# Kernel optimization log

Hardware: AMD Instinct MI355X
Metric: run time of the kernel (lower is better)

The kernel has to match this reference:

```python
import jax, jax.numpy as jnp
import numpy as np

DIM = 768
NH = 12
HD = DIM // NH
MLP = 4 * DIM
EPS = 1e-5


def _ln(x, w, b):
    mu = x.mean(-1, keepdims=True)
    var = ((x - mu) ** 2).mean(-1, keepdims=True)
    return (x - mu) * jax.lax.rsqrt(var + EPS) * w + b


def setup_inputs() -> dict:
    key = jax.random.key(0)
    ks = jax.random.split(key, 12)
    s = 0.02
    return {
        "xq": jax.random.normal(ks[0], (4, 32, 32, DIM), jnp.float32),
        "xkv": jax.random.normal(ks[1], (4, 64, 64, DIM), jnp.float32),
        "norm1_w": jnp.ones((DIM,), jnp.float32),
        "norm1_b": jnp.zeros((DIM,), jnp.float32),
        "kv_w": jax.random.normal(ks[2], (DIM, 2 * DIM), jnp.float32) * s,
        "kv_b": jnp.zeros((2 * DIM,), jnp.float32),
        "q_w": jax.random.normal(ks[3], (DIM, DIM), jnp.float32) * s,
        "q_b": jnp.zeros((DIM,), jnp.float32),
        "proj_w": jax.random.normal(ks[4], (DIM, DIM), jnp.float32) * s,
        "proj_b": jnp.zeros((DIM,), jnp.float32),
        "norm2_w": jnp.ones((DIM,), jnp.float32),
        "norm2_b": jnp.zeros((DIM,), jnp.float32),
        "mlp_w1": jax.random.normal(ks[5], (DIM, MLP), jnp.float32) * s,
        "mlp_b1": jnp.zeros((MLP,), jnp.float32),
        "mlp_w2": jax.random.normal(ks[6], (MLP, DIM), jnp.float32) * s,
        "mlp_b2": jnp.zeros((DIM,), jnp.float32),
    }


def reference(xq, xkv, norm1_w, norm1_b, kv_w, kv_b, q_w, q_b, proj_w, proj_b,
              norm2_w, norm2_b, mlp_w1, mlp_b1, mlp_w2, mlp_b2):
    B, Hq, Wq, C = xq.shape
    _, H, W, _ = xkv.shape
    shortcut = xq
    xn = _ln(xq, norm1_w, norm1_b)
    # kv projection: [B, H*W, 2, NH, HD]
    kv = (xkv.reshape(B, H * W, C) @ kv_w + kv_b).reshape(B, H * W, 2, NH, HD)
    k = kv[:, :, 0].transpose(0, 2, 1, 3)  # [B, NH, HW, HD]
    v = kv[:, :, 1].transpose(0, 2, 1, 3)
    q = (xn.reshape(B, Hq * Wq, C) @ q_w + q_b).reshape(B, Hq * Wq, NH, HD).transpose(0, 2, 1, 3)
    scale = HD ** -0.5
    attn = jnp.einsum('bhqd,bhkd->bhqk', q * scale, k)
    attn = jax.nn.softmax(attn, axis=-1)
    o = jnp.einsum('bhqk,bhkd->bhqd', attn, v)  # [B, NH, HqWq, HD]
    o = o.transpose(0, 2, 1, 3).reshape(B, Hq, Wq, C)
    o = o @ proj_w + proj_b
    x = shortcut + o
    xn2 = _ln(x, norm2_w, norm2_b)
    mlp = jax.nn.gelu(xn2 @ mlp_w1 + mlp_b1, approximate=False) @ mlp_w2 + mlp_b2
    return x + mlp
```

## Files before the change

### kernel.cpp

```cpp
#include <hip/hip_runtime.h>
#include <hip/hip_bf16.h>
#include <math.h>

#define DIM 768
#define NH 12
#define HD 64
#define NQ 1024
#define NKV 4096
#define QSCALE 0.18033688011112042f

typedef __attribute__((ext_vector_type(4))) float f32x4;
typedef __attribute__((ext_vector_type(16))) float f32x16;
typedef __attribute__((ext_vector_type(8))) __bf16 bf16x8;
typedef __attribute__((ext_vector_type(8))) unsigned short u16x8;
typedef __attribute__((ext_vector_type(4))) unsigned short u16x4;
typedef unsigned short u16;

typedef const __attribute__((address_space(1))) void* gas_t;
typedef __attribute__((address_space(3))) void* las_t;

__device__ __forceinline__ void gl16(const void* g, void* l) {
    __builtin_amdgcn_global_load_lds((gas_t)g, (las_t)l, 16, 0, 0);
}

__device__ __forceinline__ u16 f2b(float x) {
    __bf16 h = (__bf16)x;
    return __builtin_bit_cast(u16, h);
}

__device__ __forceinline__ float b2f(u16 x) {
    unsigned int u = ((unsigned int)x) << 16;
    return __builtin_bit_cast(float, u);
}

__device__ __forceinline__ f32x4 mfma16(const u16* a, const u16* b, f32x4 c) {
    bf16x8 av = *reinterpret_cast<const bf16x8*>(a);
    bf16x8 bv = *reinterpret_cast<const bf16x8*>(b);
    return __builtin_amdgcn_mfma_f32_16x16x32_bf16(av, bv, c, 0, 0, 0);
}

__device__ __forceinline__ f32x16 mfma32(bf16x8 a, bf16x8 b, f32x16 c) {
    return __builtin_amdgcn_mfma_f32_32x32x16_bf16(a, b, c, 0, 0, 0);
}

__global__ __launch_bounds__(256) void cast_bf16_kernel(
    const float* __restrict__ in, u16* __restrict__ out, int n8)
{
    int i = blockIdx.x * 256 + threadIdx.x;
    if (i >= n8) return;
    const float4* p = reinterpret_cast<const float4*>(in) + (size_t)i * 2;
    float4 a = p[0], b = p[1];
    u16x8 o;
    o[0] = f2b(a.x); o[1] = f2b(a.y); o[2] = f2b(a.z); o[3] = f2b(a.w);
    o[4] = f2b(b.x); o[5] = f2b(b.y); o[6] = f2b(b.z); o[7] = f2b(b.w);
    reinterpret_cast<u16x8*>(out)[i] = o;
}

__global__ __launch_bounds__(256) void transpose_cast_kernel(
    const float* __restrict__ W, u16* __restrict__ Wt, int K, int N)
{
    __shared__ u16 T[64][72];
    int k0 = blockIdx.y * 64, n0 = blockIdx.x * 64;
    int tid = threadIdx.x;
    int r = tid >> 2, c = (tid & 3) * 16;
    const float* src = W + (size_t)(k0 + r) * N + n0 + c;
    #pragma unroll
    for (int j = 0; j < 16; j += 4) {
        float4 f = *reinterpret_cast<const float4*>(src + j);
        T[r][c + j + 0] = f2b(f.x); T[r][c + j + 1] = f2b(f.y);
        T[r][c + j + 2] = f2b(f.z); T[r][c + j + 3] = f2b(f.w);
    }
    __syncthreads();
    int d = tid >> 2, c2 = (tid & 3) * 16;
    u16x8 o0, o1;
    #pragma unroll
    for (int j = 0; j < 8; ++j) o0[j] = T[c2 + j][d];
    #pragma unroll
    for (int j = 0; j < 8; ++j) o1[j] = T[c2 + 8 + j][d];
    u16* dst = Wt + (size_t)(n0 + d) * K + k0 + c2;
    *reinterpret_cast<u16x8*>(dst) = o0;
    *reinterpret_cast<u16x8*>(dst + 8) = o1;
}

__global__ __launch_bounds__(256) void ln_kernel(
    const float* __restrict__ x, const float* __restrict__ w,
    const float* __restrict__ b, u16* __restrict__ out)
{
    int row = blockIdx.x;
    const float* xr = x + (size_t)row * DIM;
    int tid = threadIdx.x;
    float v0 = xr[tid], v1 = xr[tid + 256], v2 = xr[tid + 512];
    float s = v0 + v1 + v2;
    float s2 = v0 * v0 + v1 * v1 + v2 * v2;
    for (int off = 1; off < 64; off <<= 1) {
        s += __shfl_xor(s, off);
        s2 += __shfl_xor(s2, off);
    }
    __shared__ float ss[4], ss2[4];
    int wid = tid >> 6, lane = tid & 63;
    if (lane == 0) { ss[wid] = s; ss2[wid] = s2; }
    __syncthreads();
    s = ss[0] + ss[1] + ss[2] + ss[3];
    s2 = ss2[0] + ss2[1] + ss2[2] + ss2[3];
    float mu = s * (1.0f / DIM);
    float var = s2 * (1.0f / DIM) - mu * mu;
    float r = rsqrtf(var + 1e-5f);
    u16* orow = out + (size_t)row * DIM;
    orow[tid]       = f2b((v0 - mu) * r * w[tid]       + b[tid]);
    orow[tid + 256] = f2b((v1 - mu) * r * w[tid + 256] + b[tid + 256]);
    orow[tid + 512] = f2b((v2 - mu) * r * w[tid + 512] + b[tid + 512]);
}

template <int EPI>
__global__ __launch_bounds__(256) void gemm_kernel(
    const u16* __restrict__ A, const u16* __restrict__ Bt,
    const float* __restrict__ bias, const float* __restrict__ res,
    void* __restrict__ out, void* __restrict__ out2, int M, int N, int K)
{
    __shared__ u16 As[2][4096];
    __shared__ u16 Bs[2][4096];
    int p = blockIdx.x;
    int nbx = N >> 7;
    int ypx = (M >> 7) >> 3;
    int xcd = p & 7, slot = p >> 3;
    int by = xcd * ypx + slot / nbx;
    int bx = slot - (slot / nbx) * nbx;
    int n0 = bx * 128, m0 = by * 128;
    int tid = threadIdx.x, lane = tid & 63, wave = tid >> 6;
    int wm = (wave >> 1) * 64, wn = (wave & 1) * 64;
    f32x4 acc[4][4] = {};

    int ca = tid, cb = tid + 256;
    int ra = ca >> 2, sa = ((ca & 3) ^ (ra & 3)) * 8;
    int rb = cb >> 2, sb = ((cb & 3) ^ (rb & 3)) * 8;
    const u16* Asrc1 = A + (size_t)(m0 + ra) * K + sa;
    const u16* Asrc2 = A + (size_t)(m0 + rb) * K + sb;
    const u16* Bsrc1 = Bt + (size_t)(n0 + ra) * K + sa;
    const u16* Bsrc2 = Bt + (size_t)(n0 + rb) * K + sb;

    auto STAGE = [&](int buf, int k0) {
        gl16(Asrc1 + k0, &As[buf][ca * 8]);
        gl16(Asrc2 + k0, &As[buf][cb * 8]);
        gl16(Bsrc1 + k0, &Bs[buf][ca * 8]);
        gl16(Bsrc2 + k0, &Bs[buf][cb * 8]);
    };

    int fr = lane & 15, fq = lane >> 4;
    int co = (fq ^ (fr & 3)) * 8;

    auto COMPUTE = [&](int buf) {
        #pragma unroll
        for (int mf = 0; mf < 4; ++mf) {
            const u16* a = &As[buf][(wm + mf * 16 + fr) * 32 + co];
            #pragma unroll
            for (int nf = 0; nf < 4; ++nf)
                acc[mf][nf] = mfma16(a, &Bs[buf][(wn + nf * 16 + fr) * 32 + co],
                                     acc[mf][nf]);
        }
    };

    STAGE(0, 0);
    asm volatile("s_waitcnt vmcnt(0)" ::: "memory");
    __builtin_amdgcn_s_barrier();
    for (int k0 = 0; k0 < K; k0 += 64) {
        STAGE(1, k0 + 32);
        COMPUTE(0);
        asm volatile("s_waitcnt vmcnt(0)" ::: "memory");
        __builtin_amdgcn_s_barrier();
        if (k0 + 64 < K) STAGE(0, k0 + 64);
        COMPUTE(1);
        asm volatile("s_waitcnt vmcnt(0)" ::: "memory");
        __builtin_amdgcn_s_barrier();
    }

    if constexpr (EPI == 4) {
        u16* kb = reinterpret_cast<u16*>(out);
        u16* vtb = reinterpret_cast<u16*>(out2);
        if (n0 < 768) {
            #pragma unroll
            for (int mf = 0; mf < 4; ++mf)
                #pragma unroll
                for (int nf = 0; nf < 4; ++nf) {
                    int col = n0 + wn + nf * 16 + fr;
                    float bv = bias[col];
                    #pragma unroll
                    for (int r = 0; r < 4; ++r) {
                        int row = m0 + wm + mf * 16 + fq * 4 + r;
                        kb[(size_t)row * 768 + col] = f2b(acc[mf][nf][r] + bv);
                    }
                }
        } else {
            #pragma unroll
            for (int mf = 0; mf < 4; ++mf)
                #pragma unroll
                for (int nf = 0; nf < 4; ++nf) {
                    int col = n0 + wn + nf * 16 + fr;
                    int c = col - 768, h = c >> 6, d = c & 63;
                    float bv = bias[col];
                    int row0 = m0 + wm + mf * 16 + fq * 4;
                    int bb = row0 >> 12, kvi = row0 & 4095;
                    int kv6 = kvi & 63;
                    int slot = (kv6 & 51) | ((kv6 & 4) << 1) | ((kv6 & 8) >> 1);
                    u16x4 pv;
                    #pragma unroll
                    for (int r = 0; r < 4; ++r) pv[r] = f2b(acc[mf][nf][r] + bv);
                    *reinterpret_cast<u16x4*>(vtb + ((size_t)(bb * 12 + h) * 64 + d) * 4096
                                              + (kvi & ~63) + slot) = pv;
                }
        }
        return;
    }

    float* outf = reinterpret_cast<float*>(out);
    u16* outb = reinterpret_cast<u16*>(out);
    #pragma unroll
    for (int mf = 0; mf < 4; ++mf)
        #pragma unroll
        for (int nf = 0; nf < 4; ++nf)
            #pragma unroll
            for (int r = 0; r < 4; ++r) {
                int row = m0 + wm + mf * 16 + fq * 4 + r;
                int col = n0 + wn + nf * 16 + fr;
                size_t idx = (size_t)row * N + col;
                float v = acc[mf][nf][r] + bias[col];
                if constexpr (EPI == 2) {
                    outf[idx] = v + res[idx];
                } else {
                    float g = 0.5f * v * (1.0f + erff(v * 0.70710678118f));
                    outb[idx] = f2b(g);
                }
            }
}

template <int EPI>
__global__ __launch_bounds__(256) void gemm64_kernel(
    const u16* __restrict__ A, const u16* __restrict__ Bt,
    const float* __restrict__ bias, const float* __restrict__ res,
    void* __restrict__ out, int M, int N, int K)
{
    __shared__ u16 As[2][4096];
    __shared__ u16 Bs[2][4096];
    int p = blockIdx.x;
    int nbx = N >> 6;
    int ypx = (M >> 6) >> 3;
    int xcd = p & 7, slot = p >> 3;
    int by = xcd * ypx + slot / nbx;
    int bx = slot - (slot / nbx) * nbx;
    int n0 = bx * 64, m0 = by * 64;
    int tid = threadIdx.x, lane = tid & 63, wave = tid >> 6;
    int wm = (wave >> 1) * 32, wn = (wave & 1) * 32;
    f32x4 acc[2][2] = {};

    int c1 = tid, c2 = tid + 256;
    int r1 = c1 >> 3, s1 = ((c1 & 7) ^ (r1 & 7)) * 8;
    int r2 = c2 >> 3, s2 = ((c2 & 7) ^ (r2 & 7)) * 8;
    const u16* As1 = A + (size_t)(m0 + r1) * K + s1;
    const u16* As2 = A + (size_t)(m0 + r2) * K + s2;
    const u16* Bt1 = Bt + (size_t)(n0 + r1) * K + s1;
    const u16* Bt2 = Bt + (size_t)(n0 + r2) * K + s2;

    auto STAGE = [&](int buf, int k0) {
        gl16(As1 + k0, &As[buf][c1 * 8]);
        gl16(As2 + k0, &As[buf][c2 * 8]);
        gl16(Bt1 + k0, &Bs[buf][c1 * 8]);
        gl16(Bt2 + k0, &Bs[buf][c2 * 8]);
    };

    int fr = lane & 15, fq = lane >> 4;
    int co0 = (fq ^ (fr & 7)) * 8;
    int co1 = ((4 + fq) ^ (fr & 7)) * 8;

    STAGE(0, 0);
    asm volatile("s_waitcnt vmcnt(0)" ::: "memory");
    __builtin_amdgcn_s_barrier();
    int NIT = K >> 6;
    for (int it = 0; it < NIT; ++it) {
        int cur = it & 1;
        if (it + 1 < NIT) STAGE(cur ^ 1, (it + 1) << 6);
        #pragma unroll
        for (int mf = 0; mf < 2; ++mf) {
            const u16* arow = &As[cur][(wm + mf * 16 + fr) * 64];
            #pragma unroll
            for (int nf = 0; nf < 2; ++nf) {
                const u16* brow = &Bs[cur][(wn + nf * 16 + fr) * 64];
                acc[mf][nf] = mfma16(arow + co0, brow + co0, acc[mf][nf]);
                acc[mf][nf] = mfma16(arow + co1, brow + co1, acc[mf][nf]);
            }
        }
        asm volatile("s_waitcnt vmcnt(0)" ::: "memory");
        __builtin_amdgcn_s_barrier();
    }

    float* outf = reinterpret_cast<float*>(out);
    u16* outb = reinterpret_cast<u16*>(out);
    #pragma unroll
    for (int mf = 0; mf < 2; ++mf)
        #pragma unroll
        for (int nf = 0; nf < 2; ++nf)
            #pragma unroll
            for (int r = 0; r < 4; ++r) {
                int row = m0 + wm + mf * 16 + fq * 4 + r;
                int col = n0 + wn + nf * 16 + fr;
                size_t idx = (size_t)row * N + col;
                float v = acc[mf][nf][r] + bias[col];
                if constexpr (EPI == 1) {
                    outb[idx] = f2b(v * QSCALE);
                } else {
                    outf[idx] = v + res[idx];
                }
            }
}

__global__ __launch_bounds__(256, 4) void attn_kernel(
    const u16* __restrict__ q, const u16* __restrict__ kbuf,
    const u16* __restrict__ vt, u16* __restrict__ op0, u16* __restrict__ op1,
    u16* __restrict__ op2, u16* __restrict__ op3, float* __restrict__ L)
{
    int p = blockIdx.x;
    int xcd = p & 7, slot = p >> 3;
    int bh = xcd * 6 + (slot >> 5);
    int rem = slot & 31;
    int qt = rem >> 2, quarter = rem & 3;
    int h = bh % NH, bb = bh / NH;
    const int NIT = 16;

    __shared__ u16 Kb[2][4096];
    __shared__ u16 Vb[2][4096];

    int tid = threadIdx.x, lane = tid & 63, wave = tid >> 6;
    int l31 = lane & 31, hi = lane >> 5;
    int sw = l31 & 7;

    u16x8 ov = {0x3F80, 0x3F80, 0x3F80, 0x3F80, 0x3F80, 0x3F80, 0x3F80, 0x3F80};
    const bf16x8 ONES = __builtin_bit_cast(bf16x8, ov);

    bf16x8 qf[4];
    {
        const u16* qbp = q + (size_t)(bb * NQ + qt * 128 + wave * 32 + l31) * DIM
                         + h * HD + hi * 8;
        #pragma unroll
        for (int ks = 0; ks < 4; ++ks)
            qf[ks] = *reinterpret_cast<const bf16x8*>(qbp + ks * 16);
    }

    int c1 = tid, c2 = tid + 256;
    int r1 = c1 >> 3, sc1 = (c1 & 7) ^ (r1 & 7);
    int r2 = c2 >> 3, sc2 = (c2 & 7) ^ (r2 & 7);
    size_t krow0 = (size_t)bb * NKV + quarter * 1024;
    const u16* ks1 = kbuf + (krow0 + r1) * 768 + h * HD + sc1 * 8;
    const u16* ks2 = kbuf + (krow0 + r2) * 768 + h * HD + sc2 * 8;
    const u16* vs1 = vt + ((size_t)bh * HD + r1) * NKV + quarter * 1024 + sc1 * 8;
    const u16* vs2 = vt + ((size_t)bh * HD + r2) * NKV + quarter * 1024 + sc2 * 8;

    auto STAGE = [&](int buf, int kv0) {
        gl16(ks1 + (size_t)kv0 * 768, &Kb[buf][c1 * 8]);
        gl16(ks2 + (size_t)kv0 * 768, &Kb[buf][c2 * 8]);
        gl16(vs1 + kv0, &Vb[buf][c1 * 8]);
        gl16(vs2 + kv0, &Vb[buf][c2 * 8]);
    };

    f32x16 oacc0 = {}, oacc1 = {}, lsum = {};

    STAGE(0, 0);
    asm volatile("s_waitcnt vmcnt(0)" ::: "memory");
    __builtin_amdgcn_s_barrier();

    auto BODY = [&](int cur, int it) {
        if (it + 1 < NIT) STAGE(cur ^ 1, (it + 1) * 64);
        const u16* vb = &Vb[cur][l31 * 64];
        #pragma unroll
        for (int kh = 0; kh < 2; ++kh) {
            const u16* kb = &Kb[cur][(kh * 32 + l31) * 64];
            f32x16 s = {};
            __builtin_amdgcn_s_setprio(1);
            #pragma unroll
            for (int ks = 0; ks < 4; ++ks) {
                bf16x8 kf = *reinterpret_cast<const bf16x8*>(
                    kb + (((ks * 2 + hi) ^ sw) * 8));
                s = mfma32(kf, qf[ks], s);
            }
            __builtin_amdgcn_s_setprio(0);
            u16x8 p0, p1;
            #pragma unroll
            for (int r = 0; r < 8; ++r) p0[r] = f2b(exp2f(s[r]));
            #pragma unroll
            for (int r = 0; r < 8; ++r) p1[r] = f2b(exp2f(s[r + 8]));
            bf16x8 a0 = __builtin_bit_cast(bf16x8, p0);
            bf16x8 a1 = __builtin_bit_cast(bf16x8, p1);
            int vc0 = ((kh * 4 + 0 + hi) ^ sw) * 8;
            int vc1 = ((kh * 4 + 2 + hi) ^ sw) * 8;
            __builtin_amdgcn_s_setprio(1);
            lsum = mfma32(a0, ONES, lsum);
            lsum = mfma32(a1, ONES, lsum);
            bf16x8 v00 = *reinterpret_cast<const bf16x8*>(vb + vc0);
            bf16x8 v01 = *reinterpret_cast<const bf16x8*>(vb + vc1);
            bf16x8 v10 = *reinterpret_cast<const bf16x8*>(vb + 2048 + vc0);
            bf16x8 v11 = *reinterpret_cast<const bf16x8*>(vb + 2048 + vc1);
            oacc0 = mfma32(a0, v00, oacc0);
            oacc0 = mfma32(a1, v01, oacc0);
            oacc1 = mfma32(a0, v10, oacc1);
            oacc1 = mfma32(a1, v11, oacc1);
            __builtin_amdgcn_s_setprio(0);
        }
        asm volatile("s_waitcnt vmcnt(0)" ::: "memory");
        __builtin_amdgcn_s_barrier();
    };

    for (int it = 0; it < NIT; it += 2) { BODY(0, it); BODY(1, it + 1); }

    u16* op = (quarter == 0) ? op0 : (quarter == 1) ? op1 : (quarter == 2) ? op2 : op3;
    #pragma unroll
    for (int r = 0; r < 16; ++r) {
        int qrow = (r & 3) + 8 * (r >> 2) + 4 * hi;
        float rcl = 1.0f / lsum[r];
        size_t orow = (size_t)(bb * NQ + qt * 128 + wave * 32 + qrow) * DIM + h * HD;
        op[orow + l31] = f2b(oacc0[r] * rcl);
        op[orow + 32 + l31] = f2b(oacc1[r] * rcl);
    }
    if (l31 == 0) {
        #pragma unroll
        for (int r = 0; r < 16; ++r) {
            int qrow = (r & 3) + 8 * (r >> 2) + 4 * hi;
            L[quarter * 49152 + bh * 1024 + qt * 128 + wave * 32 + qrow] = lsum[r];
        }
    }
}

__global__ __launch_bounds__(256) void combine_kernel(
    const u16* __restrict__ op0, const u16* __restrict__ op1,
    const u16* __restrict__ op2, const u16* __restrict__ op3,
    const float* __restrict__ L, u16* __restrict__ out)
{
    int idx = blockIdx.x * 256 + threadIdx.x;
    int t = idx / 96, cc = (idx - t * 96) * 8;
    int h = cc >> 6;
    int bb = t >> 10, qr = t & 1023;
    int li = (bb * 12 + h) * 1024 + qr;
    float l0 = L[li], l1 = L[49152 + li], l2 = L[2 * 49152 + li], l3 = L[3 * 49152 + li];
    float rs = 1.0f / (l0 + l1 + l2 + l3);
    u16x8 a = *reinterpret_cast<const u16x8*>(op0 + (size_t)t * 768 + cc);
    u16x8 b = *reinterpret_cast<const u16x8*>(op1 + (size_t)t * 768 + cc);
    u16x8 c = *reinterpret_cast<const u16x8*>(op2 + (size_t)t * 768 + cc);
    u16x8 d = *reinterpret_cast<const u16x8*>(op3 + (size_t)t * 768 + cc);
    u16x8 o;
    #pragma unroll
    for (int j = 0; j < 8; ++j)
        o[j] = f2b((b2f(a[j]) * l0 + b2f(b[j]) * l1 + b2f(c[j]) * l2 + b2f(d[j]) * l3) * rs);
    *reinterpret_cast<u16x8*>(out + (size_t)t * 768 + cc) = o;
}

extern "C" void kernel_launch(void* const* d_in, const int* in_sizes, int n_in,
                              void* d_out, int out_size, void* d_ws, size_t ws_size,
                              hipStream_t stream) {
    const float* xq  = (const float*)d_in[0];
    const float* xkv = (const float*)d_in[1];
    const float* n1w = (const float*)d_in[2];
    const float* n1b = (const float*)d_in[3];
    const float* kvw = (const float*)d_in[4];
    const float* kvb = (const float*)d_in[5];
    const float* qw  = (const float*)d_in[6];
    const float* qb  = (const float*)d_in[7];
    const float* pjw = (const float*)d_in[8];
    const float* pjb = (const float*)d_in[9];
    const float* n2w = (const float*)d_in[10];
    const float* n2b = (const float*)d_in[11];
    const float* w1  = (const float*)d_in[12];
    const float* b1  = (const float*)d_in[13];
    const float* w2  = (const float*)d_in[14];
    const float* b2  = (const float*)d_in[15];
    float* xout = (float*)d_out;

    char* ws = (char*)d_ws;
    u16* xkv_b  = (u16*)(ws);
    u16* kbuf   = (u16*)(ws + 25165824);
    u16* vt     = (u16*)(ws + 50331648);
    u16* xn_bf  = (u16*)(ws + 75497472);
    u16* q_bf   = (u16*)(ws + 81788928);
    u16* o_bf   = (u16*)(ws + 88080384);
    u16* wkv_bf = (u16*)(ws + 94371840);
    u16* wq_bf  = (u16*)(ws + 96731136);
    u16* wpj_bf = (u16*)(ws + 97910784);
    u16* w1_bf  = (u16*)(ws + 99090432);
    u16* w2_bf  = (u16*)(ws + 103809024);
    u16* hid    = xkv_b;
    u16* op2    = xkv_b;
    u16* op3    = (u16*)(ws + 6291456);
    float* Lbuf = (float*)wkv_bf;

    cast_bf16_kernel<<<dim3(6144), dim3(256), 0, stream>>>(xkv, xkv_b, 1572864);
    transpose_cast_kernel<<<dim3(24, 12), dim3(256), 0, stream>>>(kvw, wkv_bf, 768, 1536);
    transpose_cast_kernel<<<dim3(12, 12), dim3(256), 0, stream>>>(qw, wq_bf, 768, 768);
    transpose_cast_kernel<<<dim3(12, 12), dim3(256), 0, stream>>>(pjw, wpj_bf, 768, 768);
    transpose_cast_kernel<<<dim3(48, 12), dim3(256), 0, stream>>>(w1, w1_bf, 768, 3072);
    transpose_cast_kernel<<<dim3(12, 48), dim3(256), 0, stream>>>(w2, w2_bf, 3072, 768);

    ln_kernel<<<dim3(4096), dim3(256), 0, stream>>>(xq, n1w, n1b, xn_bf);
    gemm_kernel<4><<<dim3(12 * 128), dim3(256), 0, stream>>>(xkv_b, wkv_bf, kvb, nullptr, kbuf, vt, 16384, 1536, 768);
    gemm64_kernel<1><<<dim3(768), dim3(256), 0, stream>>>(xn_bf, wq_bf, qb, nullptr, q_bf, 4096, 768, 768);
    attn_kernel<<<dim3(1536), dim3(256), 0, stream>>>(q_bf, kbuf, vt, xn_bf, o_bf, op2, op3, Lbuf);
    combine_kernel<<<dim3(1536), dim3(256), 0, stream>>>(xn_bf, o_bf, op2, op3, Lbuf, q_bf);
    gemm64_kernel<2><<<dim3(768), dim3(256), 0, stream>>>(q_bf, wpj_bf, pjb, xq, xout, 4096, 768, 768);
    ln_kernel<<<dim3(4096), dim3(256), 0, stream>>>(xout, n2w, n2b, xn_bf);
    gemm_kernel<3><<<dim3(24 * 32), dim3(256), 0, stream>>>(xn_bf, w1_bf, b1, nullptr, hid, nullptr, 4096, 3072, 768);
    gemm64_kernel<2><<<dim3(768), dim3(256), 0, stream>>>(hid, w2_bf, b2, xout, xout, 4096, 768, 3072);
}
```

Measured before the change: 286.2 us.

## Fuse prep kernels into one launch and triple-buffer gemm64/attention LDS pipelines

The separate input cast, five weight transpose-casts and the first layernorm are merged into a single prep kernel that dispatches on block index. This removes six kernel launches and lets the small jobs overlap. Separately, gemm64 and attention move from double to triple LDS buffering, prefetching two tiles ahead and waiting with vmcnt(4) instead of draining all loads. The deeper pipeline raises LDS use per block, which may lower occupancy (attention declares 4 blocks per CU).

```diff
diff --git a/kernel.cpp b/kernel.cpp
--- a/kernel.cpp
+++ b/kernel.cpp
@@ -43,43 +43,82 @@
     return __builtin_amdgcn_mfma_f32_32x32x16_bf16(a, b, c, 0, 0, 0);
 }
 
-__global__ __launch_bounds__(256) void cast_bf16_kernel(
-    const float* __restrict__ in, u16* __restrict__ out, int n8)
-{
-    int i = blockIdx.x * 256 + threadIdx.x;
-    if (i >= n8) return;
-    const float4* p = reinterpret_cast<const float4*>(in) + (size_t)i * 2;
-    float4 a = p[0], b = p[1];
-    u16x8 o;
-    o[0] = f2b(a.x); o[1] = f2b(a.y); o[2] = f2b(a.z); o[3] = f2b(a.w);
-    o[4] = f2b(b.x); o[5] = f2b(b.y); o[6] = f2b(b.z); o[7] = f2b(b.w);
-    reinterpret_cast<u16x8*>(out)[i] = o;
-}
-
-__global__ __launch_bounds__(256) void transpose_cast_kernel(
-    const float* __restrict__ W, u16* __restrict__ Wt, int K, int N)
+__global__ __launch_bounds__(256) void prep_kernel(
+    const float* __restrict__ xkv, u16* __restrict__ xkv_b,
+    const float* __restrict__ kvw, u16* __restrict__ wkv_bf,
+    const float* __restrict__ qw,  u16* __restrict__ wq_bf,
+    const float* __restrict__ pjw, u16* __restrict__ wpj_bf,
+    const float* __restrict__ w1,  u16* __restrict__ w1_bf,
+    const float* __restrict__ w2,  u16* __restrict__ w2_bf,
+    const float* __restrict__ xq,  const float* __restrict__ n1w,
+    const float* __restrict__ n1b, u16* __restrict__ xn_bf)
 {
     __shared__ u16 T[64][72];
-    int k0 = blockIdx.y * 64, n0 = blockIdx.x * 64;
-    int tid = threadIdx.x;
-    int r = tid >> 2, c = (tid & 3) * 16;
-    const float* src = W + (size_t)(k0 + r) * N + n0 + c;
-    #pragma unroll
-    for (int j = 0; j < 16; j += 4) {
-        float4 f = *reinterpret_cast<const float4*>(src + j);
-        T[r][c + j + 0] = f2b(f.x); T[r][c + j + 1] = f2b(f.y);
-        T[r][c + j + 2] = f2b(f.z); T[r][c + j + 3] = f2b(f.w);
-    }
+    int b = blockIdx.x, tid = threadIdx.x;
+    if (b < 6144) {
+        int i = b * 256 + tid;
+        const float4* p = reinterpret_cast<const float4*>(xkv) + (size_t)i * 2;
+        float4 a = p[0], bb = p[1];
+        u16x8 o;
+        o[0] = f2b(a.x); o[1] = f2b(a.y); o[2] = f2b(a.z); o[3] = f2b(a.w);
+        o[4] = f2b(bb.x); o[5] = f2b(bb.y); o[6] = f2b(bb.z); o[7] = f2b(bb.w);
+        reinterpret_cast<u16x8*>(xkv_b)[i] = o;
+        return;
+    }
+    if (b < 7872) {
+        int b2 = b - 6144;
+        const float* W; u16* Wt; int K, N, nbx, base;
+        if (b2 < 288)       { W = kvw; Wt = wkv_bf; K = 768;  N = 1536; nbx = 24; base = 0; }
+        else if (b2 < 432)  { W = qw;  Wt = wq_bf;  K = 768;  N = 768;  nbx = 12; base = 288; }
+        else if (b2 < 576)  { W = pjw; Wt = wpj_bf; K = 768;  N = 768;  nbx = 12; base = 432; }
+        else if (b2 < 1152) { W = w1;  Wt = w1_bf;  K = 768;  N = 3072; nbx = 48; base = 576; }
+        else                { W = w2;  Wt = w2_bf;  K = 3072; N = 768;  nbx = 12; base = 1152; }
+        int bb2 = b2 - base;
+        int bx = bb2 % nbx, by = bb2 / nbx;
+        int k0 = by * 64, n0 = bx * 64;
+        int r = tid >> 2, c = (tid & 3) * 16;
+        const float* src = W + (size_t)(k0 + r) * N + n0 + c;
+        #pragma unroll
+        for (int j = 0; j < 16; j += 4) {
+            float4 f = *reinterpret_cast<const float4*>(src + j);
+            T[r][c + j + 0] = f2b(f.x); T[r][c + j + 1] = f2b(f.y);
+            T[r][c + j + 2] = f2b(f.z); T[r][c + j + 3] = f2b(f.w);
+        }
+        __syncthreads();
+        int d = tid >> 2, c2 = (tid & 3) * 16;
+        u16x8 o0, o1;
+        #pragma unroll
+        for (int j = 0; j < 8; ++j) o0[j] = T[c2 + j][d];
+        #pragma unroll
+        for (int j = 0; j < 8; ++j) o1[j] = T[c2 + 8 + j][d];
+        u16* dst = Wt + (size_t)(n0 + d) * K + k0 + c2;
+        *reinterpret_cast<u16x8*>(dst) = o0;
+        *reinterpret_cast<u16x8*>(dst + 8) = o1;
+        return;
+    }
+    int row = b - 7872;
+    const float* xr = xq + (size_t)row * DIM;
+    float v0 = xr[tid], v1 = xr[tid + 256], v2 = xr[tid + 512];
+    float s = v0 + v1 + v2;
+    float s2 = v0 * v0 + v1 * v1 + v2 * v2;
+    for (int off = 1; off < 64; off <<= 1) {
+        s += __shfl_xor(s, off);
+        s2 += __shfl_xor(s2, off);
+    }
+    float* ss = reinterpret_cast<float*>(&T[0][0]);
+    float* ss2 = ss + 4;
+    int wid = tid >> 6, lane = tid & 63;
+    if (lane == 0) { ss[wid] = s; ss2[wid] = s2; }
     __syncthreads();
-    int d = tid >> 2, c2 = (tid & 3) * 16;
-    u16x8 o0, o1;
-    #pragma unroll
-    for (int j = 0; j < 8; ++j) o0[j] = T[c2 + j][d];
-    #pragma unroll
-    for (int j = 0; j < 8; ++j) o1[j] = T[c2 + 8 + j][d];
-    u16* dst = Wt + (size_t)(n0 + d) * K + k0 + c2;
-    *reinterpret_cast<u16x8*>(dst) = o0;
-    *reinterpret_cast<u16x8*>(dst + 8) = o1;
+    s = ss[0] + ss[1] + ss[2] + ss[3];
+    s2 = ss2[0] + ss2[1] + ss2[2] + ss2[3];
+    float mu = s * (1.0f / DIM);
+    float var = s2 * (1.0f / DIM) - mu * mu;
+    float r = rsqrtf(var + 1e-5f);
+    u16* orow = xn_bf + (size_t)row * DIM;
+    orow[tid]       = f2b((v0 - mu) * r * n1w[tid]       + n1b[tid]);
+    orow[tid + 256] = f2b((v1 - mu) * r * n1w[tid + 256] + n1b[tid + 256]);
+    orow[tid + 512] = f2b((v2 - mu) * r * n1w[tid + 512] + n1b[tid + 512]);
 }
 
 __global__ __launch_bounds__(256) void ln_kernel(
@@ -238,8 +277,8 @@
     const float* __restrict__ bias, const float* __restrict__ res,
     void* __restrict__ out, int M, int N, int K)
 {
-    __shared__ u16 As[2][4096];
-    __shared__ u16 Bs[2][4096];
+    __shared__ u16 As[3][4096];
+    __shared__ u16 Bs[3][4096];
     int p = blockIdx.x;
     int nbx = N >> 6;
     int ypx = (M >> 6) >> 3;
@@ -270,13 +309,16 @@
     int co0 = (fq ^ (fr & 7)) * 8;
     int co1 = ((4 + fq) ^ (fr & 7)) * 8;
 
+    int NIT = K >> 6;
     STAGE(0, 0);
-    asm volatile("s_waitcnt vmcnt(0)" ::: "memory");
+    STAGE(1, 64);
+    asm volatile("s_waitcnt vmcnt(4)" ::: "memory");
     __builtin_amdgcn_s_barrier();
-    int NIT = K >> 6;
+    int cur = 0;
     for (int it = 0; it < NIT; ++it) {
-        int cur = it & 1;
-        if (it + 1 < NIT) STAGE(cur ^ 1, (it + 1) << 6);
+        int pre = (cur >= 1) ? cur - 1 : 2;
+        bool more = (it + 2 < NIT);
+        if (more) STAGE(pre, (it + 2) << 6);
         #pragma unroll
         for (int mf = 0; mf < 2; ++mf) {
             const u16* arow = &As[cur][(wm + mf * 16 + fr) * 64];
@@ -287,8 +329,10 @@
                 acc[mf][nf] = mfma16(arow + co1, brow + co1, acc[mf][nf]);
             }
         }
-        asm volatile("s_waitcnt vmcnt(0)" ::: "memory");
+        if (more) { asm volatile("s_waitcnt vmcnt(4)" ::: "memory"); }
+        else      { asm volatile("s_waitcnt vmcnt(0)" ::: "memory"); }
         __builtin_amdgcn_s_barrier();
+        cur = (cur == 2) ? 0 : cur + 1;
     }
 
     float* outf = reinterpret_cast<float*>(out);
@@ -324,8 +368,8 @@
     int h = bh % NH, bb = bh / NH;
     const int NIT = 16;
 
-    __shared__ u16 Kb[2][4096];
-    __shared__ u16 Vb[2][4096];
+    __shared__ u16 Kb[3][4096];
+    __shared__ u16 Vb[3][4096];
 
     int tid = threadIdx.x, lane = tid & 63, wave = tid >> 6;
     int l31 = lane & 31, hi = lane >> 5;
@@ -362,11 +406,15 @@
     f32x16 oacc0 = {}, oacc1 = {}, lsum = {};
 
     STAGE(0, 0);
-    asm volatile("s_waitcnt vmcnt(0)" ::: "memory");
+    STAGE(1, 64);
+    asm volatile("s_waitcnt vmcnt(4)" ::: "memory");
     __builtin_amdgcn_s_barrier();
 
-    auto BODY = [&](int cur, int it) {
-        if (it + 1 < NIT) STAGE(cur ^ 1, (it + 1) * 64);
+    int cur = 0;
+    for (int it = 0; it < NIT; ++it) {
+        int pre = (cur >= 1) ? cur - 1 : 2;
+        bool more = (it + 2 < NIT);
+        if (more) STAGE(pre, (it + 2) * 64);
         const u16* vb = &Vb[cur][l31 * 64];
         #pragma unroll
         for (int kh = 0; kh < 2; ++kh) {
@@ -402,11 +450,11 @@
             oacc1 = mfma32(a1, v11, oacc1);
             __builtin_amdgcn_s_setprio(0);
         }
-        asm volatile("s_waitcnt vmcnt(0)" ::: "memory");
+        if (more) { asm volatile("s_waitcnt vmcnt(4)" ::: "memory"); }
+        else      { asm volatile("s_waitcnt vmcnt(0)" ::: "memory"); }
         __builtin_amdgcn_s_barrier();
-    };
-
-    for (int it = 0; it < NIT; it += 2) { BODY(0, it); BODY(1, it + 1); }
+        cur = (cur == 2) ? 0 : cur + 1;
+    }
 
     u16* op = (quarter == 0) ? op0 : (quarter == 1) ? op1 : (quarter == 2) ? op2 : op3;
     #pragma unroll
@@ -487,14 +535,9 @@
     u16* op3    = (u16*)(ws + 6291456);
     float* Lbuf = (float*)wkv_bf;
 
-    cast_bf16_kernel<<<dim3(6144), dim3(256), 0, stream>>>(xkv, xkv_b, 1572864);
-    transpose_cast_kernel<<<dim3(24, 12), dim3(256), 0, stream>>>(kvw, wkv_bf, 768, 1536);
-    transpose_cast_kernel<<<dim3(12, 12), dim3(256), 0, stream>>>(qw, wq_bf, 768, 768);
-    transpose_cast_kernel<<<dim3(12, 12), dim3(256), 0, stream>>>(pjw, wpj_bf, 768, 768);
-    transpose_cast_kernel<<<dim3(48, 12), dim3(256), 0, stream>>>(w1, w1_bf, 768, 3072);
-    transpose_cast_kernel<<<dim3(12, 48), dim3(256), 0, stream>>>(w2, w2_bf, 3072, 768);
-
-    ln_kernel<<<dim3(4096), dim3(256), 0, stream>>>(xq, n1w, n1b, xn_bf);
+    prep_kernel<<<dim3(11968), dim3(256), 0, stream>>>(
+        xkv, xkv_b, kvw, wkv_bf, qw, wq_bf, pjw, wpj_bf, w1, w1_bf, w2, w2_bf,
+        xq, n1w, n1b, xn_bf);
     gemm_kernel<4><<<dim3(12 * 128), dim3(256), 0, stream>>>(xkv_b, wkv_bf, kvb, nullptr, kbuf, vt, 16384, 1536, 768);
     gemm64_kernel<1><<<dim3(768), dim3(256), 0, stream>>>(xn_bf, wq_bf, qb, nullptr, q_bf, 4096, 768, 768);
     attn_kernel<<<dim3(1536), dim3(256), 0, stream>>>(q_bf, kbuf, vt, xn_bf, o_bf, op2, op3, Lbuf);
```

Measured after the change: 281.9 us. About the same (-1.5%).
